# Performance work log

Hardware: AMD Instinct MI355X
Metric: run time of the kernel (lower is better)

Reference implementation:

```python
import jax, jax.numpy as jnp
import numpy as np

TEMPERATURE = 0.07
NEG_INF = -1e9
EPS = 1e-12  # matches F.normalize eps

B, N, D = 512, 128, 512


def _l2norm(x):
    return x / jnp.maximum(jnp.linalg.norm(x, axis=-1, keepdims=True), EPS)


def setup_inputs() -> dict:
    key = jax.random.key(0)
    k1, k2, k3, k4 = jax.random.split(key, 4)
    text_embeddings = jax.random.normal(k1, (B, D), dtype=jnp.float32)
    all_visual_embeddings = jax.random.normal(k2, (B, N, D), dtype=jnp.float32)
    valid = jax.random.bernoulli(k3, 0.9, (B, N))
    gt_indices = jax.random.randint(k4, (B,), 0, N, dtype=jnp.int64 if jax.config.jax_enable_x64 else jnp.int32)
    return {
        'text_embeddings': text_embeddings,
        'all_visual_embeddings': all_visual_embeddings,
        'valid': valid,
        'gt_indices': gt_indices,
    }


def reference(text_embeddings, all_visual_embeddings, valid, gt_indices):
    Bb, Nn, Dd = all_visual_embeddings.shape
    tn = _l2norm(text_embeddings)                 # (B, D)
    vn = _l2norm(all_visual_embeddings)           # (B, N, D)

    gt_c = jnp.clip(gt_indices, 0, Nn - 1)
    barange = jnp.arange(Bb)
    gt_vis = vn[barange, gt_c]                    # (B, D) GT visual per sample
    sample_valid = (gt_indices >= 0) & (gt_indices < Nn) & valid[barange, gt_c]  # (B,)

    pos_sim = jnp.sum(tn * gt_vis, axis=-1) / TEMPERATURE            # (B,)

    # in-sample hard negatives: all valid humans except GT
    sims_in = jnp.einsum('bd,bnd->bn', tn, vn) / TEMPERATURE          # (B, N)
    in_mask = valid & (jnp.arange(Nn)[None, :] != gt_c[:, None])      # (B, N)

    # in-batch negatives: other samples' valid GT visuals
    sims_batch = (tn @ gt_vis.T) / TEMPERATURE                        # (B, B)
    batch_mask = sample_valid[None, :] & ~jnp.eye(Bb, dtype=bool)     # (B, B)

    neg_logits = jnp.concatenate([
        jnp.where(in_mask, sims_in, NEG_INF),
        jnp.where(batch_mask, sims_batch, NEG_INF),
    ], axis=1)                                                        # (B, N+B)

    # CE with label 0 over [pos, negs] = logsumexp - pos
    lse = jax.nn.logsumexp(jnp.concatenate([pos_sim[:, None], neg_logits], axis=1), axis=1)
    loss_per = lse - pos_sim                                          # (B,)

    has_neg = jnp.any(in_mask, axis=1) | jnp.any(batch_mask, axis=1)
    contrib = sample_valid & has_neg
    n_valid = jnp.sum(sample_valid.astype(jnp.float32))
    denom = jnp.maximum(n_valid, 1.0)

    total = jnp.sum(jnp.where(contrib, loss_per, 0.0)) / denom
    max_neg = jnp.max(neg_logits, axis=1)
    correct = contrib & (pos_sim >= max_neg)  # argmax ties go to index 0 (pos)
    accuracy = jnp.sum(correct.astype(jnp.float32)) / denom
    return total, accuracy
```

## Files before the change

kernel.cpp:

```cpp
#include <hip/hip_runtime.h>
#include <hip/hip_bf16.h>
#include <math.h>

constexpr int B_ = 512;
constexpr int N_ = 128;
constexpr int D_ = 512;
constexpr float TEMP_INV = 1.0f / 0.07f;
constexpr float NEG_INF_ = -1e9f;
constexpr float EPS_ = 1e-12f;

constexpr size_t OFF_TN   = 0;
constexpr size_t OFF_GTV  = OFF_TN + (size_t)B_ * D_;
constexpr size_t OFF_POS  = OFF_GTV + (size_t)B_ * D_;
constexpr size_t OFF_LIN  = OFF_POS + B_;
constexpr size_t OFF_LB   = OFF_LIN + (size_t)B_ * N_;
constexpr size_t OFF_SV   = OFF_LB + (size_t)B_ * B_;
constexpr size_t OFF_V8   = OFF_SV + B_;
constexpr size_t OFF_SCAL = OFF_V8 + (size_t)B_ * N_ / 4;

__device__ __forceinline__ float wave_sum(float v) {
    for (int off = 32; off; off >>= 1) v += __shfl_xor(v, off);
    return v;
}

__global__ __launch_bounds__(256) void detect_kernel(const unsigned int* __restrict__ w,
                                                     int* __restrict__ flags) {
    int i = blockIdx.x * blockDim.x + threadIdx.x;
    unsigned int v = w[i];
    unsigned long long mf = __ballot(v == 0x3f800000u);
    unsigned long long mb = __ballot((v & 0xffffff00u) != 0u);
    if ((threadIdx.x & 63) == 0) {
        if (mf) atomicOr(&flags[0], 1);
        if (mb) atomicOr(&flags[1], 1);
    }
}

__global__ __launch_bounds__(256) void convert_valid_kernel(const void* __restrict__ raw,
                                                            const int* __restrict__ flags,
                                                            unsigned char* __restrict__ out) {
    int i = blockIdx.x * blockDim.x + threadIdx.x;
    if (i >= B_ * N_) return;
    unsigned char v;
    if (flags[0])      v = (((const float*)raw)[i] != 0.0f) ? 1 : 0;
    else if (flags[1]) v = (((const unsigned char*)raw)[i] != 0) ? 1 : 0;
    else               v = (((const int*)raw)[i] != 0) ? 1 : 0;
    out[i] = v;
}

__global__ __launch_bounds__(256) void phaseA_kernel(const float* __restrict__ text,
                                                     const float* __restrict__ visual,
                                                     const int* __restrict__ gt,
                                                     const unsigned char* __restrict__ valid8,
                                                     float* __restrict__ tn,
                                                     float* __restrict__ gtv,
                                                     float* __restrict__ pos_sim,
                                                     int* __restrict__ svalid,
                                                     int* __restrict__ n_valid) {
    int b = blockIdx.x;
    int tid = threadIdx.x;
    int g = gt[b];
    int gc = min(max(g, 0), N_ - 1);
    const float* trow = text + (size_t)b * D_;
    const float* vrow = visual + ((size_t)b * N_ + gc) * D_;
    float t0 = trow[tid], t1 = trow[tid + 256];
    float v0 = vrow[tid], v1 = vrow[tid + 256];
    float sst = t0 * t0 + t1 * t1;
    float ssv = v0 * v0 + v1 * v1;
    float dot = t0 * v0 + t1 * v1;
    sst = wave_sum(sst);
    ssv = wave_sum(ssv);
    dot = wave_sum(dot);
    __shared__ float r0[4], r1[4], r2[4];
    __shared__ float invt_sh, invv_sh;
    int wave = tid >> 6, lane = tid & 63;
    if (lane == 0) { r0[wave] = sst; r1[wave] = ssv; r2[wave] = dot; }
    __syncthreads();
    if (tid == 0) {
        float st = r0[0] + r0[1] + r0[2] + r0[3];
        float sv = r1[0] + r1[1] + r1[2] + r1[3];
        float d  = r2[0] + r2[1] + r2[2] + r2[3];
        float invt = 1.0f / fmaxf(sqrtf(st), EPS_);
        float invv = 1.0f / fmaxf(sqrtf(sv), EPS_);
        invt_sh = invt;
        invv_sh = invv;
        pos_sim[b] = d * invt * invv * TEMP_INV;
        int s = (g >= 0 && g < N_ && valid8[(size_t)b * N_ + gc]) ? 1 : 0;
        svalid[b] = s;
        if (s) atomicAdd(n_valid, 1);
    }
    __syncthreads();
    float invt = invt_sh, invv = invv_sh;
    tn [(size_t)b * D_ + tid]       = t0 * invt;
    tn [(size_t)b * D_ + tid + 256] = t1 * invt;
    gtv[(size_t)b * D_ + tid]       = v0 * invv;
    gtv[(size_t)b * D_ + tid + 256] = v1 * invv;
}

__global__ __launch_bounds__(256) void insample_kernel(const float* __restrict__ visual,
                                                       const float* __restrict__ tn,
                                                       const int* __restrict__ gt,
                                                       const unsigned char* __restrict__ valid8,
                                                       float* __restrict__ logits_in) {
    int bid = blockIdx.x;
    int b = bid >> 2;
    int tile = bid & 3;
    int tid = threadIdx.x;
    __shared__ float4 tsh4[D_ / 4];
    if (tid < 128) tsh4[tid] = ((const float4*)(tn + (size_t)b * D_))[tid];
    __syncthreads();
    int g = gt[b];
    int gc = min(max(g, 0), N_ - 1);
    int wave = tid >> 6, lane = tid & 63;
    int sub = lane >> 4;
    int s = lane & 15;
    #pragma unroll
    for (int p = 0; p < 2; ++p) {
        int n = tile * 32 + p * 16 + wave * 4 + sub;
        const float4* vrow = (const float4*)(visual + ((size_t)b * N_ + n) * D_);
        float dot = 0.0f, ss = 0.0f;
        #pragma unroll
        for (int it = 0; it < 8; ++it) {
            float4 v = vrow[s + 16 * it];
            float4 t = tsh4[s + 16 * it];
            dot += v.x * t.x + v.y * t.y + v.z * t.z + v.w * t.w;
            ss  += v.x * v.x + v.y * v.y + v.z * v.z + v.w * v.w;
        }
        #pragma unroll
        for (int off = 8; off; off >>= 1) {
            dot += __shfl_xor(dot, off);
            ss  += __shfl_xor(ss, off);
        }
        if (s == 0) {
            bool m = valid8[(size_t)b * N_ + n] && (n != gc);
            float inv = 1.0f / fmaxf(sqrtf(ss), EPS_);
            logits_in[(size_t)b * N_ + n] = m ? dot * inv * TEMP_INV : NEG_INF_;
        }
    }
}

__global__ __launch_bounds__(256) void batch_kernel(const float* __restrict__ gtv,
                                                    const float* __restrict__ tn,
                                                    const int* __restrict__ svalid,
                                                    float* __restrict__ lb) {
    int bid = blockIdx.x;
    int b0 = (bid >> 2) * 4;
    int jbase = (bid & 3) * 128;
    int tid = threadIdx.x;
    __shared__ float4 tsh4[4 * (D_ / 4)];
    #pragma unroll
    for (int idx = tid; idx < 4 * (D_ / 4); idx += 256) {
        int r = idx >> 7, c = idx & 127;
        tsh4[idx] = ((const float4*)tn)[(size_t)(b0 + r) * (D_ / 4) + c];
    }
    __syncthreads();
    int wave = tid >> 6, lane = tid & 63;
    int sub = lane >> 4;
    int s = lane & 15;
    #pragma unroll
    for (int p = 0; p < 8; ++p) {
        int j = jbase + p * 16 + wave * 4 + sub;
        const float4* grow = (const float4*)gtv + (size_t)j * (D_ / 4);
        float a0 = 0.0f, a1 = 0.0f, a2 = 0.0f, a3 = 0.0f;
        #pragma unroll
        for (int it = 0; it < 8; ++it) {
            float4 v  = grow[s + 16 * it];
            float4 t0 = tsh4[0 * 128 + s + 16 * it];
            float4 t1 = tsh4[1 * 128 + s + 16 * it];
            float4 t2 = tsh4[2 * 128 + s + 16 * it];
            float4 t3 = tsh4[3 * 128 + s + 16 * it];
            a0 += v.x * t0.x + v.y * t0.y + v.z * t0.z + v.w * t0.w;
            a1 += v.x * t1.x + v.y * t1.y + v.z * t1.z + v.w * t1.w;
            a2 += v.x * t2.x + v.y * t2.y + v.z * t2.z + v.w * t2.w;
            a3 += v.x * t3.x + v.y * t3.y + v.z * t3.z + v.w * t3.w;
        }
        #pragma unroll
        for (int off = 8; off; off >>= 1) {
            a0 += __shfl_xor(a0, off);
            a1 += __shfl_xor(a1, off);
            a2 += __shfl_xor(a2, off);
            a3 += __shfl_xor(a3, off);
        }
        int sv = svalid[j];
        if (s < 4) {
            float av = (s == 0) ? a0 : (s == 1) ? a1 : (s == 2) ? a2 : a3;
            int brow = b0 + s;
            lb[(size_t)brow * B_ + j] = (sv && j != brow) ? av * TEMP_INV : NEG_INF_;
        }
    }
}

__global__ __launch_bounds__(256) void lse_kernel(const float* __restrict__ logits_in,
                                                  const float* __restrict__ lb,
                                                  const float* __restrict__ pos_sim,
                                                  const int* __restrict__ svalid,
                                                  float* __restrict__ accum) {
    int b = blockIdx.x;
    int tid = threadIdx.x;
    float pos = pos_sim[b];
    float x0 = (tid < N_) ? logits_in[(size_t)b * N_ + tid]
                          : lb[(size_t)b * B_ + (tid - N_)];
    float x1 = lb[(size_t)b * B_ + (tid + 256 - N_)];
    float x2 = (tid < N_) ? lb[(size_t)b * B_ + (tid + 512 - N_)] : NEG_INF_;
    float lmax = fmaxf(fmaxf(x0, x1), x2);
    for (int off = 32; off; off >>= 1) lmax = fmaxf(lmax, __shfl_xor(lmax, off));
    __shared__ float red[4];
    __shared__ float sh1;
    int wave = tid >> 6, lane = tid & 63;
    if (lane == 0) red[wave] = lmax;
    __syncthreads();
    if (tid == 0) sh1 = fmaxf(fmaxf(red[0], red[1]), fmaxf(red[2], red[3]));
    __syncthreads();
    float maxneg = sh1;
    float m = fmaxf(maxneg, pos);
    float lsum = __expf(x0 - m) + __expf(x1 - m) + ((tid < N_) ? __expf(x2 - m) : 0.0f);
    lsum = wave_sum(lsum);
    __syncthreads();
    if (lane == 0) red[wave] = lsum;
    __syncthreads();
    if (tid == 0) {
        float sum = red[0] + red[1] + red[2] + red[3] + __expf(pos - m);
        float lse = m + logf(sum);
        float loss = lse - pos;
        bool has_neg = maxneg > -1e8f;
        bool contrib = (svalid[b] != 0) && has_neg;
        if (contrib) {
            atomicAdd(&accum[0], loss);
            if (pos >= maxneg) atomicAdd(&accum[1], 1.0f);
        }
    }
}

__global__ void finalize_kernel(const float* __restrict__ accum,
                                const int* __restrict__ n_valid,
                                float* __restrict__ out) {
    if (threadIdx.x == 0 && blockIdx.x == 0) {
        float denom = fmaxf((float)(*n_valid), 1.0f);
        out[0] = accum[0] / denom;
        out[1] = accum[1] / denom;
    }
}

extern "C" void kernel_launch(void* const* d_in, const int* in_sizes, int n_in,
                              void* d_out, int out_size, void* d_ws, size_t ws_size,
                              hipStream_t stream) {
    const float* text   = (const float*)d_in[0];
    const float* visual = (const float*)d_in[1];
    const void*  valid  = d_in[2];
    const int*   gt     = (const int*)d_in[3];
    float* out = (float*)d_out;

    float* wsf = (float*)d_ws;
    float* tn      = wsf + OFF_TN;
    float* gtv     = wsf + OFF_GTV;
    float* pos_sim = wsf + OFF_POS;
    float* lin     = wsf + OFF_LIN;
    float* lb      = wsf + OFF_LB;
    int*   svalid  = (int*)(wsf + OFF_SV);
    unsigned char* valid8 = (unsigned char*)(wsf + OFF_V8);
    int*   flags   = (int*)(wsf + OFF_SCAL);
    int*   n_valid = (int*)(wsf + OFF_SCAL) + 2;
    float* accum   = (wsf + OFF_SCAL) + 3;

    hipMemsetAsync(wsf + OFF_SCAL, 0, 5 * sizeof(float), stream);

    detect_kernel<<<64, 256, 0, stream>>>((const unsigned int*)valid, flags);
    convert_valid_kernel<<<(B_ * N_ + 255) / 256, 256, 0, stream>>>(valid, flags, valid8);
    phaseA_kernel<<<B_, 256, 0, stream>>>(text, visual, gt, valid8, tn, gtv, pos_sim, svalid, n_valid);
    insample_kernel<<<B_ * 4, 256, 0, stream>>>(visual, tn, gt, valid8, lin);
    batch_kernel<<<B_, 256, 0, stream>>>(gtv, tn, svalid, lb);
    lse_kernel<<<B_, 256, 0, stream>>>(lin, lb, pos_sim, svalid, accum);
    finalize_kernel<<<1, 64, 0, stream>>>(accum, n_valid, out);
}
```

Baseline: 235.3 us.

## Fuse valid conversion, normalization and GT extraction into in-sample kernel

Removes the separate valid-conversion and phaseA kernels. The in-sample kernel now normalizes text per block, decodes the validity mask inline, and has the GT row's wave produce pos_sim, svalid and the normalized GT visual. The finalize kernel is folded into the LSE kernel through a last-block-done atomic counter. This cuts launches and avoids a second read of the GT visual rows, in exchange for recomputing the text norm in all four tile blocks and relying on the counter-based completion pattern.

```diff
diff --git a/kernel.cpp b/kernel.cpp
--- a/kernel.cpp
+++ b/kernel.cpp
@@ -15,8 +15,7 @@
 constexpr size_t OFF_LIN  = OFF_POS + B_;
 constexpr size_t OFF_LB   = OFF_LIN + (size_t)B_ * N_;
 constexpr size_t OFF_SV   = OFF_LB + (size_t)B_ * B_;
-constexpr size_t OFF_V8   = OFF_SV + B_;
-constexpr size_t OFF_SCAL = OFF_V8 + (size_t)B_ * N_ / 4;
+constexpr size_t OFF_SCAL = OFF_SV + B_;
 
 __device__ __forceinline__ float wave_sum(float v) {
     for (int off = 32; off; off >>= 1) v += __shfl_xor(v, off);
@@ -35,84 +34,56 @@
     }
 }
 
-__global__ __launch_bounds__(256) void convert_valid_kernel(const void* __restrict__ raw,
-                                                            const int* __restrict__ flags,
-                                                            unsigned char* __restrict__ out) {
-    int i = blockIdx.x * blockDim.x + threadIdx.x;
-    if (i >= B_ * N_) return;
-    unsigned char v;
-    if (flags[0])      v = (((const float*)raw)[i] != 0.0f) ? 1 : 0;
-    else if (flags[1]) v = (((const unsigned char*)raw)[i] != 0) ? 1 : 0;
-    else               v = (((const int*)raw)[i] != 0) ? 1 : 0;
-    out[i] = v;
-}
-
-__global__ __launch_bounds__(256) void phaseA_kernel(const float* __restrict__ text,
-                                                     const float* __restrict__ visual,
-                                                     const int* __restrict__ gt,
-                                                     const unsigned char* __restrict__ valid8,
-                                                     float* __restrict__ tn,
-                                                     float* __restrict__ gtv,
-                                                     float* __restrict__ pos_sim,
-                                                     int* __restrict__ svalid,
-                                                     int* __restrict__ n_valid) {
-    int b = blockIdx.x;
-    int tid = threadIdx.x;
-    int g = gt[b];
-    int gc = min(max(g, 0), N_ - 1);
-    const float* trow = text + (size_t)b * D_;
-    const float* vrow = visual + ((size_t)b * N_ + gc) * D_;
-    float t0 = trow[tid], t1 = trow[tid + 256];
-    float v0 = vrow[tid], v1 = vrow[tid + 256];
-    float sst = t0 * t0 + t1 * t1;
-    float ssv = v0 * v0 + v1 * v1;
-    float dot = t0 * v0 + t1 * v1;
-    sst = wave_sum(sst);
-    ssv = wave_sum(ssv);
-    dot = wave_sum(dot);
-    __shared__ float r0[4], r1[4], r2[4];
-    __shared__ float invt_sh, invv_sh;
-    int wave = tid >> 6, lane = tid & 63;
-    if (lane == 0) { r0[wave] = sst; r1[wave] = ssv; r2[wave] = dot; }
-    __syncthreads();
-    if (tid == 0) {
-        float st = r0[0] + r0[1] + r0[2] + r0[3];
-        float sv = r1[0] + r1[1] + r1[2] + r1[3];
-        float d  = r2[0] + r2[1] + r2[2] + r2[3];
-        float invt = 1.0f / fmaxf(sqrtf(st), EPS_);
-        float invv = 1.0f / fmaxf(sqrtf(sv), EPS_);
-        invt_sh = invt;
-        invv_sh = invv;
-        pos_sim[b] = d * invt * invv * TEMP_INV;
-        int s = (g >= 0 && g < N_ && valid8[(size_t)b * N_ + gc]) ? 1 : 0;
-        svalid[b] = s;
-        if (s) atomicAdd(n_valid, 1);
-    }
-    __syncthreads();
-    float invt = invt_sh, invv = invv_sh;
-    tn [(size_t)b * D_ + tid]       = t0 * invt;
-    tn [(size_t)b * D_ + tid + 256] = t1 * invt;
-    gtv[(size_t)b * D_ + tid]       = v0 * invv;
-    gtv[(size_t)b * D_ + tid + 256] = v1 * invv;
-}
-
-__global__ __launch_bounds__(256) void insample_kernel(const float* __restrict__ visual,
-                                                       const float* __restrict__ tn,
-                                                       const int* __restrict__ gt,
-                                                       const unsigned char* __restrict__ valid8,
-                                                       float* __restrict__ logits_in) {
+__device__ __forceinline__ int decode_valid(const void* raw, int f0, int f1, size_t idx) {
+    if (f0) return ((const float*)raw)[idx] != 0.0f;
+    if (f1) return ((const unsigned char*)raw)[idx] != 0;
+    return ((const int*)raw)[idx] != 0;
+}
+
+__global__ __launch_bounds__(256) void fused_insample_kernel(
+        const float* __restrict__ text,
+        const float* __restrict__ visual,
+        const int* __restrict__ gt,
+        const void* __restrict__ valid_raw,
+        const int* __restrict__ flags,
+        float* __restrict__ tn,
+        float* __restrict__ gtv,
+        float* __restrict__ pos_sim,
+        int* __restrict__ svalid,
+        int* __restrict__ n_valid,
+        float* __restrict__ lin) {
     int bid = blockIdx.x;
     int b = bid >> 2;
     int tile = bid & 3;
     int tid = threadIdx.x;
+    int f0 = flags[0], f1 = flags[1];
+
     __shared__ float4 tsh4[D_ / 4];
-    if (tid < 128) tsh4[tid] = ((const float4*)(tn + (size_t)b * D_))[tid];
-    __syncthreads();
+    float* tshf = (float*)tsh4;
+    const float* trow = text + (size_t)b * D_;
+    float t0 = trow[tid], t1 = trow[tid + 256];
+    float sst = wave_sum(t0 * t0 + t1 * t1);
+    __shared__ float red[4];
+    __shared__ float invt_sh;
+    int wave = tid >> 6, lane = tid & 63;
+    if (lane == 0) red[wave] = sst;
+    __syncthreads();
+    if (tid == 0) invt_sh = 1.0f / fmaxf(sqrtf(red[0] + red[1] + red[2] + red[3]), EPS_);
+    __syncthreads();
+    float invt = invt_sh;
+    t0 *= invt; t1 *= invt;
+    tshf[tid] = t0; tshf[tid + 256] = t1;
+    if (tile == 0) {
+        tn[(size_t)b * D_ + tid]       = t0;
+        tn[(size_t)b * D_ + tid + 256] = t1;
+    }
+    __syncthreads();
+
     int g = gt[b];
     int gc = min(max(g, 0), N_ - 1);
-    int wave = tid >> 6, lane = tid & 63;
     int sub = lane >> 4;
     int s = lane & 15;
+
     #pragma unroll
     for (int p = 0; p < 2; ++p) {
         int n = tile * 32 + p * 16 + wave * 4 + sub;
@@ -130,10 +101,25 @@
             dot += __shfl_xor(dot, off);
             ss  += __shfl_xor(ss, off);
         }
+        float inv = 1.0f / fmaxf(sqrtf(ss), EPS_);
         if (s == 0) {
-            bool m = valid8[(size_t)b * N_ + n] && (n != gc);
-            float inv = 1.0f / fmaxf(sqrtf(ss), EPS_);
-            logits_in[(size_t)b * N_ + n] = m ? dot * inv * TEMP_INV : NEG_INF_;
+            int vb = decode_valid(valid_raw, f0, f1, (size_t)b * N_ + n);
+            bool m = vb && (n != gc);
+            lin[(size_t)b * N_ + n] = m ? dot * inv * TEMP_INV : NEG_INF_;
+            if (n == gc) {
+                pos_sim[b] = dot * inv * TEMP_INV;
+                int sv = (g >= 0 && g < N_ && vb) ? 1 : 0;
+                svalid[b] = sv;
+                if (sv) atomicAdd(n_valid, 1);
+            }
+        }
+        if (n == gc) {
+            float4* gdst = (float4*)(gtv + (size_t)b * D_);
+            #pragma unroll
+            for (int it = 0; it < 8; ++it) {
+                float4 v = vrow[s + 16 * it];
+                gdst[s + 16 * it] = make_float4(v.x * inv, v.y * inv, v.z * inv, v.w * inv);
+            }
         }
     }
 }
@@ -193,7 +179,10 @@
                                                   const float* __restrict__ lb,
                                                   const float* __restrict__ pos_sim,
                                                   const int* __restrict__ svalid,
-                                                  float* __restrict__ accum) {
+                                                  float* __restrict__ accum,
+                                                  int* __restrict__ n_valid,
+                                                  int* __restrict__ done,
+                                                  float* __restrict__ out) {
     int b = blockIdx.x;
     int tid = threadIdx.x;
     float pos = pos_sim[b];
@@ -227,16 +216,16 @@
             atomicAdd(&accum[0], loss);
             if (pos >= maxneg) atomicAdd(&accum[1], 1.0f);
         }
-    }
-}
-
-__global__ void finalize_kernel(const float* __restrict__ accum,
-                                const int* __restrict__ n_valid,
-                                float* __restrict__ out) {
-    if (threadIdx.x == 0 && blockIdx.x == 0) {
-        float denom = fmaxf((float)(*n_valid), 1.0f);
-        out[0] = accum[0] / denom;
-        out[1] = accum[1] / denom;
+        __threadfence();
+        int prev = atomicAdd(done, 1);
+        if (prev == B_ - 1) {
+            float total = atomicAdd(&accum[0], 0.0f);
+            float acc   = atomicAdd(&accum[1], 0.0f);
+            int   nv    = atomicAdd(n_valid, 0);
+            float denom = fmaxf((float)nv, 1.0f);
+            out[0] = total / denom;
+            out[1] = acc / denom;
+        }
     }
 }
 
@@ -256,18 +245,16 @@
     float* lin     = wsf + OFF_LIN;
     float* lb      = wsf + OFF_LB;
     int*   svalid  = (int*)(wsf + OFF_SV);
-    unsigned char* valid8 = (unsigned char*)(wsf + OFF_V8);
     int*   flags   = (int*)(wsf + OFF_SCAL);
     int*   n_valid = (int*)(wsf + OFF_SCAL) + 2;
     float* accum   = (wsf + OFF_SCAL) + 3;
-
-    hipMemsetAsync(wsf + OFF_SCAL, 0, 5 * sizeof(float), stream);
+    int*   done    = (int*)(wsf + OFF_SCAL) + 5;
+
+    hipMemsetAsync(wsf + OFF_SCAL, 0, 6 * sizeof(float), stream);
 
     detect_kernel<<<64, 256, 0, stream>>>((const unsigned int*)valid, flags);
-    convert_valid_kernel<<<(B_ * N_ + 255) / 256, 256, 0, stream>>>(valid, flags, valid8);
-    phaseA_kernel<<<B_, 256, 0, stream>>>(text, visual, gt, valid8, tn, gtv, pos_sim, svalid, n_valid);
-    insample_kernel<<<B_ * 4, 256, 0, stream>>>(visual, tn, gt, valid8, lin);
+    fused_insample_kernel<<<B_ * 4, 256, 0, stream>>>(text, visual, gt, valid, flags,
+                                                      tn, gtv, pos_sim, svalid, n_valid, lin);
     batch_kernel<<<B_, 256, 0, stream>>>(gtv, tn, svalid, lb);
-    lse_kernel<<<B_, 256, 0, stream>>>(lin, lb, pos_sim, svalid, accum);
-    finalize_kernel<<<1, 64, 0, stream>>>(accum, n_valid, out);
-}
+    lse_kernel<<<B_, 256, 0, stream>>>(lin, lb, pos_sim, svalid, accum, n_valid, done, out);
+}
```

After: 233.7 us. About the same (-0.7%).
